# Optimization experiments

Hardware: AMD Instinct MI355X
Metric: run time of the kernel (lower is better)

The kernel has to match this reference:

```python
import jax, jax.numpy as jnp
import numpy as np

S, O, H = 8, 1024, 1024
B, N = 32, 512

def setup_inputs() -> dict:
    key = jax.random.key(0)
    k1, k2, k3, k4 = jax.random.split(key, 4)
    x = jax.random.normal(k1, (B, N, H), dtype=jnp.float32)
    subject_id = jax.random.randint(k2, (B,), 0, S)
    # kaiming_uniform_(a=sqrt(5)) on [S,O,H]: fan_in=H, gain=sqrt(2/(1+5)), bound=gain*sqrt(3/fan_in)
    wbound = jnp.sqrt(2.0 / 6.0) * jnp.sqrt(3.0 / H)
    weight = jax.random.uniform(k3, (S, O, H), minval=-wbound, maxval=wbound, dtype=jnp.float32)
    bbound = 1.0 / jnp.sqrt(H)
    bias = jax.random.uniform(k4, (S, O), minval=-bbound, maxval=bbound, dtype=jnp.float32)
    return {"x": x, "subject_id": subject_id, "weight": weight, "bias": bias}

def reference(x, subject_id, weight, bias):
    # Per-sample weight gather + batched matmul + bias add
    W = weight[subject_id]          # [B, O, H]
    b = bias[subject_id]            # [B, O]
    y = jnp.einsum('bnh,boh->bno', x, W) + b[:, None, :]
    return y
```

## Files before the change

### kernel.cpp

```cpp
#include <hip/hip_runtime.h>


constexpr int S_DIM = 8;
constexpr int O_DIM = 1024;
constexpr int H_DIM = 1024;
constexpr int B_DIM = 32;
constexpr int N_DIM = 512;

constexpr int BM = 128;
constexpr int BN = 128;
constexpr int BK = 64;
constexpr int NTHREADS = 256;

constexpr long long X_ELEMS = (long long)B_DIM * N_DIM * H_DIM;
constexpr long long W_ELEMS = (long long)S_DIM * O_DIM * H_DIM;
constexpr size_t XB_BYTES = (size_t)X_ELEMS * 2;

typedef short bf16x8 __attribute__((ext_vector_type(8)));
typedef float f32x4 __attribute__((ext_vector_type(4)));
typedef float f32x2 __attribute__((ext_vector_type(2)));
typedef __bf16 bf16x2 __attribute__((ext_vector_type(2)));

__device__ __forceinline__ unsigned int cvt_pk_bf16(float a, float b) {
  f32x2 v;
  v[0] = a;
  v[1] = b;
  bf16x2 r = __builtin_convertvector(v, bf16x2);
  return __builtin_bit_cast(unsigned int, r);
}

__device__ __forceinline__ void gload_lds16(const void* g, void* l) {
  __builtin_amdgcn_global_load_lds(
      (const __attribute__((address_space(1))) unsigned int*)g,
      (__attribute__((address_space(3))) unsigned int*)l, 16, 0, 0);
}

__global__ __launch_bounds__(256) void cvt_kernel(
    const float* __restrict__ x, const float* __restrict__ w,
    unsigned short* __restrict__ xb, unsigned short* __restrict__ wb) {
  const int blk = blockIdx.x;
  const float* src;
  unsigned short* dst;
  long long base;
  if (blk < 4096) {
    src = x; dst = xb; base = (long long)blk * 4096;
  } else {
    src = w; dst = wb; base = (long long)(blk - 4096) * 4096;
  }
  const long long e0 = base + threadIdx.x * 4;
#pragma unroll
  for (int c = 0; c < 4; ++c) {
    const f32x4 v = __builtin_nontemporal_load((const f32x4*)(src + e0 + c * 1024));
    uint2 u;
    u.x = cvt_pk_bf16(v[0], v[1]);
    u.y = cvt_pk_bf16(v[2], v[3]);
    *(uint2*)(dst + e0 + c * 1024) = u;
  }
}

__global__ __launch_bounds__(NTHREADS, 4) void scl_gemm(
    const unsigned short* __restrict__ xb, const int* __restrict__ subject_id,
    const unsigned short* __restrict__ wb, const float* __restrict__ bias,
    float* __restrict__ out) {
  __shared__ __align__(16) unsigned short As[BM * BK];
  __shared__ __align__(16) unsigned short Bs[BN * BK];

  const int tid = threadIdx.x;
  const int b = blockIdx.z;
  const int n0 = blockIdx.x * BM;
  const int o0 = blockIdx.y * BN;
  const int sid = subject_id[b];

  const int lane = tid & 63;
  const int wid = tid >> 6;
  const int wm0 = (wid >> 1) * 64;
  const int wn0 = (wid & 1) * 64;
  const int lcol = lane & 15;
  const int lq = lane >> 4;

  const int rl = lane >> 3;
  const int srow = wid * 32 + rl;
  const int skc = ((lane & 7) ^ rl) * 8;
  const unsigned short* ag = xb + (size_t)(b * N_DIM + n0 + srow) * H_DIM + skc;
  const unsigned short* bg = wb + (size_t)(sid * O_DIM + o0 + srow) * H_DIM + skc;
  unsigned short* as_base = &As[(wid * 32) * BK];
  unsigned short* bs_base = &Bs[(wid * 32) * BK];

  f32x4 acc[4][4];
#pragma unroll
  for (int mi = 0; mi < 4; ++mi)
#pragma unroll
    for (int ni = 0; ni < 4; ++ni) {
      f32x4 z = {0.f, 0.f, 0.f, 0.f};
      acc[mi][ni] = z;
    }

  for (int k0 = 0; k0 < H_DIM; k0 += BK) {
    __syncthreads();
#pragma unroll
    for (int i = 0; i < 4; ++i) {
      gload_lds16(ag + (size_t)(i * 8) * H_DIM + k0, as_base + i * 8 * BK);
      gload_lds16(bg + (size_t)(i * 8) * H_DIM + k0, bs_base + i * 8 * BK);
    }
    __syncthreads();

#pragma unroll
    for (int kk = 0; kk < BK; kk += 32) {
      const int clog = (kk >> 3) + lq;
      bf16x8 af[4], bfr[4];
#pragma unroll
      for (int mi = 0; mi < 4; ++mi) {
        const int ar = wm0 + mi * 16 + lcol;
        af[mi] = *(const bf16x8*)(&As[ar * BK + ((clog ^ (ar & 7)) << 3)]);
      }
#pragma unroll
      for (int ni = 0; ni < 4; ++ni) {
        const int br = wn0 + ni * 16 + lcol;
        bfr[ni] = *(const bf16x8*)(&Bs[br * BK + ((clog ^ (br & 7)) << 3)]);
      }
#pragma unroll
      for (int mi = 0; mi < 4; ++mi)
#pragma unroll
        for (int ni = 0; ni < 4; ++ni)
          acc[mi][ni] = __builtin_amdgcn_mfma_f32_16x16x32_bf16(
              af[mi], bfr[ni], acc[mi][ni], 0, 0, 0);
    }
  }

  float bv[4];
#pragma unroll
  for (int ni = 0; ni < 4; ++ni)
    bv[ni] = bias[sid * O_DIM + o0 + wn0 + ni * 16 + lcol];

  float* outb = out + (size_t)(b * N_DIM + n0 + wm0) * O_DIM + o0 + wn0 + lcol;
#pragma unroll
  for (int mi = 0; mi < 4; ++mi) {
#pragma unroll
    for (int r = 0; r < 4; ++r) {
      float* orow = outb + (size_t)(mi * 16 + lq * 4 + r) * O_DIM;
#pragma unroll
      for (int ni = 0; ni < 4; ++ni)
        orow[ni * 16] = acc[mi][ni][r] + bv[ni];
    }
  }
}

extern "C" void kernel_launch(void* const* d_in, const int* in_sizes, int n_in,
                              void* d_out, int out_size, void* d_ws, size_t ws_size,
                              hipStream_t stream) {
  const float* x = (const float*)d_in[0];
  const int* subject_id = (const int*)d_in[1];
  const float* weight = (const float*)d_in[2];
  const float* bias = (const float*)d_in[3];
  float* out = (float*)d_out;

  unsigned short* xb = (unsigned short*)d_ws;
  unsigned short* wb = (unsigned short*)((char*)d_ws + XB_BYTES);

  cvt_kernel<<<6144, 256, 0, stream>>>(x, weight, xb, wb);

  dim3 grid(N_DIM / BM, O_DIM / BN, B_DIM);
  scl_gemm<<<grid, NTHREADS, 0, stream>>>(xb, subject_id, wb, bias, out);
}
```

Baseline: 182.4 us.

## Use 256x256 tiles with 8 waves and double-buffered LDS pipeline

```diff
diff --git a/kernel.cpp b/kernel.cpp
--- a/kernel.cpp
+++ b/kernel.cpp
@@ -7,13 +7,12 @@
 constexpr int B_DIM = 32;
 constexpr int N_DIM = 512;
 
-constexpr int BM = 128;
-constexpr int BN = 128;
+constexpr int BM = 256;
+constexpr int BN = 256;
 constexpr int BK = 64;
-constexpr int NTHREADS = 256;
+constexpr int NKT = H_DIM / BK;
 
 constexpr long long X_ELEMS = (long long)B_DIM * N_DIM * H_DIM;
-constexpr long long W_ELEMS = (long long)S_DIM * O_DIM * H_DIM;
 constexpr size_t XB_BYTES = (size_t)X_ELEMS * 2;
 
 typedef short bf16x8 __attribute__((ext_vector_type(8)));
@@ -58,83 +57,185 @@
   }
 }
 
-__global__ __launch_bounds__(NTHREADS, 4) void scl_gemm(
+#define BAR() __builtin_amdgcn_s_barrier()
+#define VMW(N) asm volatile("s_waitcnt vmcnt(" #N ")" ::: "memory")
+#define LGKM0()                                            \
+  do {                                                     \
+    asm volatile("s_waitcnt lgkmcnt(0)" ::: "memory");     \
+    __builtin_amdgcn_sched_barrier(0);                     \
+  } while (0)
+
+#define LDA4(ABUF, MB)                                                   \
+  do {                                                                   \
+    _Pragma("unroll") for (int m_ = 0; m_ < 4; ++m_) {                   \
+      const int ar_ = wr * 128 + ((MB) + m_) * 16 + lcol;                \
+      const unsigned short* ap_ = (ABUF) + ar_ * BK;                     \
+      af[m_][0] = *(const bf16x8*)(ap_ + (pc0 << 3));                    \
+      af[m_][1] = *(const bf16x8*)(ap_ + ((pc0 ^ 4) << 3));              \
+    }                                                                    \
+  } while (0)
+
+#define LDB2(BBUF, NB)                                                   \
+  do {                                                                   \
+    _Pragma("unroll") for (int n_ = 0; n_ < 2; ++n_) {                   \
+      const int br_ = wc * 64 + ((NB) + n_) * 16 + lcol;                 \
+      const unsigned short* bp_ = (BBUF) + br_ * BK;                     \
+      bfr[n_][0] = *(const bf16x8*)(bp_ + (pc0 << 3));                   \
+      bfr[n_][1] = *(const bf16x8*)(bp_ + ((pc0 ^ 4) << 3));             \
+    }                                                                    \
+  } while (0)
+
+#define MM4(MB, NB)                                                         \
+  do {                                                                      \
+    _Pragma("unroll") for (int m_ = 0; m_ < 4; ++m_)                        \
+    _Pragma("unroll") for (int n_ = 0; n_ < 2; ++n_)                        \
+    _Pragma("unroll") for (int x_ = 0; x_ < 2; ++x_)                        \
+      acc[(MB) + m_][(NB) + n_] = __builtin_amdgcn_mfma_f32_16x16x32_bf16(  \
+          af[m_][x_], bfr[n_][x_], acc[(MB) + m_][(NB) + n_], 0, 0, 0);     \
+  } while (0)
+
+#define STAGE_A(H, DST, KT)                                                 \
+  do {                                                                      \
+    gload_lds16(agA + (size_t)((H) * 64) * H_DIM + (KT) * 64,               \
+                (DST) + ((H) * 64 + wid * 8) * BK);                         \
+    gload_lds16(agA + (size_t)((H) * 64 + 128) * H_DIM + (KT) * 64,         \
+                (DST) + ((H) * 64 + 128 + wid * 8) * BK);                   \
+  } while (0)
+
+#define STAGE_B(S, DST, KT)                                                 \
+  do {                                                                      \
+    gload_lds16(bgB0 + (size_t)((S) * 32) * H_DIM + (KT) * 64,              \
+                (DST) + (bq0 + (S) * 32) * BK);                             \
+    gload_lds16(bgB1 + (size_t)((S) * 32) * H_DIM + (KT) * 64,              \
+                (DST) + (bq1 + (S) * 32) * BK);                             \
+  } while (0)
+
+__global__ __launch_bounds__(512, 2) void scl_gemm(
     const unsigned short* __restrict__ xb, const int* __restrict__ subject_id,
     const unsigned short* __restrict__ wb, const float* __restrict__ bias,
     float* __restrict__ out) {
-  __shared__ __align__(16) unsigned short As[BM * BK];
-  __shared__ __align__(16) unsigned short Bs[BN * BK];
+  __shared__ __align__(16) unsigned short As[2][BM * BK];
+  __shared__ __align__(16) unsigned short Bs[2][BN * BK];
 
   const int tid = threadIdx.x;
-  const int b = blockIdx.z;
-  const int n0 = blockIdx.x * BM;
-  const int o0 = blockIdx.y * BN;
-  const int sid = subject_id[b];
-
   const int lane = tid & 63;
   const int wid = tid >> 6;
-  const int wm0 = (wid >> 1) * 64;
-  const int wn0 = (wid & 1) * 64;
+  const int wr = wid >> 2;
+  const int wc = wid & 3;
   const int lcol = lane & 15;
   const int lq = lane >> 4;
-
   const int rl = lane >> 3;
-  const int srow = wid * 32 + rl;
-  const int skc = ((lane & 7) ^ rl) * 8;
-  const unsigned short* ag = xb + (size_t)(b * N_DIM + n0 + srow) * H_DIM + skc;
-  const unsigned short* bg = wb + (size_t)(sid * O_DIM + o0 + srow) * H_DIM + skc;
-  unsigned short* as_base = &As[(wid * 32) * BK];
-  unsigned short* bs_base = &Bs[(wid * 32) * BK];
-
-  f32x4 acc[4][4];
-#pragma unroll
-  for (int mi = 0; mi < 4; ++mi)
+  const int pc0 = lq ^ (lane & 7);
+
+  const int bid = blockIdx.x;
+  const int b = (bid & 7) * 4 + ((bid >> 3) & 3);
+  const int t = bid >> 5;
+  const int n0 = (t & 1) * BM;
+  const int o0 = (t >> 1) * BN;
+  const int sid = subject_id[b];
+
+  const int skc = ((lane & 7) ^ rl) << 3;
+  const unsigned short* agA =
+      xb + (size_t)(b * N_DIM + n0 + wid * 8 + rl) * H_DIM + skc;
+  const int bq0 = ((wid * 2) >> 2) * 64 + ((wid * 2) & 3) * 8;
+  const int bq1 = ((wid * 2 + 1) >> 2) * 64 + ((wid * 2 + 1) & 3) * 8;
+  const unsigned short* bgB0 =
+      wb + (size_t)(sid * O_DIM + o0 + bq0 + rl) * H_DIM + skc;
+  const unsigned short* bgB1 =
+      wb + (size_t)(sid * O_DIM + o0 + bq1 + rl) * H_DIM + skc;
+
+  unsigned short* const As0 = &As[0][0];
+  unsigned short* const As1 = &As[1][0];
+  unsigned short* const Bs0 = &Bs[0][0];
+  unsigned short* const Bs1 = &Bs[1][0];
+
+  f32x4 acc[8][4];
+#pragma unroll
+  for (int mi = 0; mi < 8; ++mi)
 #pragma unroll
     for (int ni = 0; ni < 4; ++ni) {
       f32x4 z = {0.f, 0.f, 0.f, 0.f};
       acc[mi][ni] = z;
     }
 
-  for (int k0 = 0; k0 < H_DIM; k0 += BK) {
-    __syncthreads();
-#pragma unroll
-    for (int i = 0; i < 4; ++i) {
-      gload_lds16(ag + (size_t)(i * 8) * H_DIM + k0, as_base + i * 8 * BK);
-      gload_lds16(bg + (size_t)(i * 8) * H_DIM + k0, bs_base + i * 8 * BK);
-    }
-    __syncthreads();
-
-#pragma unroll
-    for (int kk = 0; kk < BK; kk += 32) {
-      const int clog = (kk >> 3) + lq;
-      bf16x8 af[4], bfr[4];
-#pragma unroll
-      for (int mi = 0; mi < 4; ++mi) {
-        const int ar = wm0 + mi * 16 + lcol;
-        af[mi] = *(const bf16x8*)(&As[ar * BK + ((clog ^ (ar & 7)) << 3)]);
-      }
-#pragma unroll
-      for (int ni = 0; ni < 4; ++ni) {
-        const int br = wn0 + ni * 16 + lcol;
-        bfr[ni] = *(const bf16x8*)(&Bs[br * BK + ((clog ^ (br & 7)) << 3)]);
-      }
-#pragma unroll
-      for (int mi = 0; mi < 4; ++mi)
-#pragma unroll
-        for (int ni = 0; ni < 4; ++ni)
-          acc[mi][ni] = __builtin_amdgcn_mfma_f32_16x16x32_bf16(
-              af[mi], bfr[ni], acc[mi][ni], 0, 0, 0);
-    }
+  bf16x8 af[4][2];
+  bfr_decl:;
+  bf16x8 bfr[2][2];
+
+  STAGE_A(0, As0, 0);
+  STAGE_B(0, Bs0, 0);
+  STAGE_A(1, As0, 0);
+  STAGE_B(1, Bs0, 0);
+  STAGE_A(0, As1, 1);
+  STAGE_B(0, Bs1, 1);
+  VMW(8);
+  BAR();
+
+#pragma unroll
+  for (int kt = 0; kt < NKT; ++kt) {
+    unsigned short* const Ac = (kt & 1) ? As1 : As0;
+    unsigned short* const Bc = (kt & 1) ? Bs1 : Bs0;
+    unsigned short* const Ao = (kt & 1) ? As0 : As1;
+    unsigned short* const Bo = (kt & 1) ? Bs0 : Bs1;
+
+    LDA4(Ac, 0);
+    LDB2(Bc, 0);
+    if (kt + 1 < NKT) {
+      STAGE_A(1, Ao, kt + 1);
+      VMW(6);
+    } else {
+      VMW(0);
+    }
+    BAR();
+    LGKM0();
+    __builtin_amdgcn_s_setprio(1);
+    MM4(0, 0);
+    __builtin_amdgcn_s_setprio(0);
+    BAR();
+
+    LDB2(Bc, 2);
+    if (kt + 1 < NKT) STAGE_B(1, Bo, kt + 1);
+    BAR();
+    LGKM0();
+    __builtin_amdgcn_s_setprio(1);
+    MM4(0, 2);
+    __builtin_amdgcn_s_setprio(0);
+    BAR();
+
+    LDA4(Ac, 4);
+    LDB2(Bc, 0);
+    if (kt + 2 < NKT) STAGE_A(0, Ac, kt + 2);
+    BAR();
+    LGKM0();
+    __builtin_amdgcn_s_setprio(1);
+    MM4(4, 0);
+    __builtin_amdgcn_s_setprio(0);
+    BAR();
+
+    LDB2(Bc, 2);
+    if (kt + 2 < NKT) {
+      STAGE_B(0, Bc, kt + 2);
+      VMW(8);
+    } else if (kt + 2 == NKT) {
+      VMW(4);
+    }
+    BAR();
+    LGKM0();
+    __builtin_amdgcn_s_setprio(1);
+    MM4(4, 2);
+    __builtin_amdgcn_s_setprio(0);
+    BAR();
   }
 
   float bv[4];
 #pragma unroll
   for (int ni = 0; ni < 4; ++ni)
-    bv[ni] = bias[sid * O_DIM + o0 + wn0 + ni * 16 + lcol];
-
-  float* outb = out + (size_t)(b * N_DIM + n0 + wm0) * O_DIM + o0 + wn0 + lcol;
-#pragma unroll
-  for (int mi = 0; mi < 4; ++mi) {
+    bv[ni] = bias[sid * O_DIM + o0 + wc * 64 + ni * 16 + lcol];
+
+  float* outb =
+      out + (size_t)(b * N_DIM + n0 + wr * 128) * O_DIM + o0 + wc * 64 + lcol;
+#pragma unroll
+  for (int mi = 0; mi < 8; ++mi) {
 #pragma unroll
     for (int r = 0; r < 4; ++r) {
       float* orow = outb + (size_t)(mi * 16 + lq * 4 + r) * O_DIM;
@@ -159,6 +260,5 @@
 
   cvt_kernel<<<6144, 256, 0, stream>>>(x, weight, xb, wb);
 
-  dim3 grid(N_DIM / BM, O_DIM / BN, B_DIM);
-  scl_gemm<<<grid, NTHREADS, 0, stream>>>(xb, subject_id, wb, bias, out);
-}
+  scl_gemm<<<256, 512, 0, stream>>>(xb, subject_id, wb, bias, out);
+}
```

New measurement: 179.3 us. No clear change (-1.7%).
